# Optimization experiments

Measured on AMD Instinct MI355X. Metric: run time of the kernel, lower is better.

## Reference

```python
import jax, jax.numpy as jnp
import numpy as np

D_MODEL = 1024
N_HEADS = 16
HEAD_DIM = D_MODEL // N_HEADS
FFN_DIM = 4096
T = 2048
LN_EPS = 1e-5


def layer_norm(x, g, b):
    mu = jnp.mean(x, axis=-1, keepdims=True)
    var = jnp.mean(jnp.square(x - mu), axis=-1, keepdims=True)
    return (x - mu) * jax.lax.rsqrt(var + LN_EPS) * g + b


def setup_inputs() -> dict:
    key = jax.random.key(0)
    ks = jax.random.split(key, 12)
    s = 0.02
    x = jax.random.normal(ks[0], (1, T, D_MODEL), dtype=jnp.float32)
    # causal mask: True means masked (strict upper triangle)
    causal_mask = jnp.triu(jnp.ones((T, T), dtype=bool), k=1)
    # ALiBi bias: -slope * distance, per head
    slopes = 2.0 ** (-8.0 * (jnp.arange(1, N_HEADS + 1, dtype=jnp.float32) / N_HEADS))
    pos = jnp.arange(T, dtype=jnp.float32)
    dist = pos[None, :] - pos[:, None]  # (T, T)
    alibi_bias = slopes[:, None, None] * jnp.minimum(dist, 0.0)[None]  # (H, T, T)
    inp = {
        "x": x,
        "causal_mask": causal_mask,
        "alibi_bias": alibi_bias.astype(jnp.float32),
        "wq": jax.random.normal(ks[1], (D_MODEL, D_MODEL), jnp.float32) * s,
        "bq": jnp.zeros((D_MODEL,), jnp.float32),
        "wk": jax.random.normal(ks[2], (D_MODEL, D_MODEL), jnp.float32) * s,
        "bk": jnp.zeros((D_MODEL,), jnp.float32),
        "wv": jax.random.normal(ks[3], (D_MODEL, D_MODEL), jnp.float32) * s,
        "bv": jnp.zeros((D_MODEL,), jnp.float32),
        "wo": jax.random.normal(ks[4], (D_MODEL, D_MODEL), jnp.float32) * s,
        "bo": jnp.zeros((D_MODEL,), jnp.float32),
        "w1": jax.random.normal(ks[5], (D_MODEL, FFN_DIM), jnp.float32) * s,
        "b1": jnp.zeros((FFN_DIM,), jnp.float32),
        "w2": jax.random.normal(ks[6], (FFN_DIM, D_MODEL), jnp.float32) * s,
        "b2": jnp.zeros((D_MODEL,), jnp.float32),
        "g1": jnp.ones((D_MODEL,), jnp.float32),
        "be1": jnp.zeros((D_MODEL,), jnp.float32),
        "g2": jnp.ones((D_MODEL,), jnp.float32),
        "be2": jnp.zeros((D_MODEL,), jnp.float32),
    }
    return inp


def reference(x, causal_mask, alibi_bias, wq, bq, wk, bk, wv, bv, wo, bo,
              w1, b1, w2, b2, g1, be1, g2, be2):
    B, Tt, D = x.shape
    H, hd = N_HEADS, HEAD_DIM
    x_norm = layer_norm(x, g1, be1)
    # projections -> (B, H, T, hd)
    def split_heads(y):
        return y.reshape(B, Tt, H, hd).transpose(0, 2, 1, 3)
    Q = split_heads(x_norm @ wq + bq)
    K = split_heads(x_norm @ wk + bk)
    V = split_heads(x_norm @ wv + bv)
    scale = jnp.sqrt(jnp.float32(hd))
    scores = jnp.einsum('bhqd,bhkd->bhqk', Q, K) / scale
    scores = scores + alibi_bias[None]
    scores = jnp.where(causal_mask[None, None], -jnp.inf, scores)
    attn = jax.nn.softmax(scores, axis=-1)
    attn_out = jnp.einsum('bhqk,bhkd->bhqd', attn, V)
    attn_out = attn_out.transpose(0, 2, 1, 3).reshape(B, Tt, D)
    attn_out = attn_out @ wo + bo
    x = x + attn_out
    x_norm = layer_norm(x, g2, be2)
    h = jax.nn.gelu(x_norm @ w1 + b1, approximate=False)
    ffn_out = h @ w2 + b2
    return x + ffn_out
```

## Files before the change

kernel.cpp:

```cpp
#include <hip/hip_runtime.h>
#include <hip/hip_bf16.h>
#include <math.h>

#define T_SEQ 2048
#define D_MODEL 1024
#define N_HEADS 16
#define HEAD_DIM 64
#define FFN_DIM 4096

typedef _Float16 halfx8 __attribute__((ext_vector_type(8)));
typedef _Float16 halfx4 __attribute__((ext_vector_type(4)));
typedef float floatx4 __attribute__((ext_vector_type(4)));

__device__ __forceinline__ void async_ld16(const _Float16* g, _Float16* l) {
  __builtin_amdgcn_global_load_lds(
      (const __attribute__((address_space(1))) unsigned int*)g,
      (__attribute__((address_space(3))) unsigned int*)l, 16, 0, 0);
}

__global__ __launch_bounds__(256) void ln_h_kernel(
    const float* __restrict__ x, const float* __restrict__ g,
    const float* __restrict__ b, _Float16* __restrict__ y) {
  int row = blockIdx.x;
  const float* xr = x + (size_t)row * D_MODEL;
  _Float16* yr = y + (size_t)row * D_MODEL;
  int tid = threadIdx.x;
  int lid = tid & 63, wid = tid >> 6;
  __shared__ float red[8];

  float4 v = *(const float4*)&xr[tid * 4];
  float sum = v.x + v.y + v.z + v.w;
  for (int o = 32; o > 0; o >>= 1) sum += __shfl_down(sum, o, 64);
  if (lid == 0) red[wid] = sum;
  __syncthreads();
  if (tid == 0) { float t = 0; for (int i = 0; i < 4; i++) t += red[i]; red[0] = t; }
  __syncthreads();
  float mu = red[0] * (1.0f / D_MODEL);
  __syncthreads();

  float dx = v.x - mu, dy = v.y - mu, dz = v.z - mu, dw = v.w - mu;
  float vs = dx * dx + dy * dy + dz * dz + dw * dw;
  for (int o = 32; o > 0; o >>= 1) vs += __shfl_down(vs, o, 64);
  if (lid == 0) red[wid] = vs;
  __syncthreads();
  if (tid == 0) { float t = 0; for (int i = 0; i < 4; i++) t += red[i]; red[0] = t; }
  __syncthreads();
  float rstd = rsqrtf(red[0] * (1.0f / D_MODEL) + 1e-5f);

  float4 gv = *(const float4*)&g[tid * 4];
  float4 bv = *(const float4*)&b[tid * 4];
  halfx4 o;
  o[0] = (_Float16)(dx * rstd * gv.x + bv.x);
  o[1] = (_Float16)(dy * rstd * gv.y + bv.y);
  o[2] = (_Float16)(dz * rstd * gv.z + bv.z);
  o[3] = (_Float16)(dw * rstd * gv.w + bv.w);
  *(halfx4*)&yr[tid * 4] = o;
}

__global__ __launch_bounds__(256) void prep_kernel(
    const float* __restrict__ wq, const float* __restrict__ wk,
    const float* __restrict__ wv, const float* __restrict__ wo,
    const float* __restrict__ w1, const float* __restrict__ w2,
    const float* __restrict__ bq, const float* __restrict__ bk,
    const float* __restrict__ bv, _Float16* __restrict__ Wqkvt,
    _Float16* __restrict__ Wot, _Float16* __restrict__ W1t,
    _Float16* __restrict__ W2t, float* __restrict__ bqkv) {
  int bId = blockIdx.x;
  int tid = threadIdx.x;
  if (bId >= 12288) {
    int i = (bId - 12288) * 256 + tid;
    if (i < 1024) bqkv[i] = bq[i];
    else if (i < 2048) bqkv[i] = bk[i - 1024];
    else bqkv[i] = bv[i - 2048];
    return;
  }
  const float* in; _Float16* outp; int K, N, t;
  if (bId < 1024)      { in = wq; outp = Wqkvt;                 K = 1024; N = 1024; t = bId; }
  else if (bId < 2048) { in = wk; outp = Wqkvt + 1024 * 1024;   K = 1024; N = 1024; t = bId - 1024; }
  else if (bId < 3072) { in = wv; outp = Wqkvt + 2 * 1024 * 1024; K = 1024; N = 1024; t = bId - 2048; }
  else if (bId < 4096) { in = wo; outp = Wot;                   K = 1024; N = 1024; t = bId - 3072; }
  else if (bId < 8192) { in = w1; outp = W1t;                   K = 1024; N = 4096; t = bId - 4096; }
  else                 { in = w2; outp = W2t;                   K = 4096; N = 1024; t = bId - 8192; }
  int ntn = N / 32;
  int tk = (t / ntn) * 32, tn = (t % ntn) * 32;

  __shared__ float tile[32][33];
  int r = tid >> 3, c = (tid & 7) * 4;
  float4 v = *(const float4*)&in[(size_t)(tk + r) * N + tn + c];
  tile[r][c] = v.x; tile[r][c + 1] = v.y; tile[r][c + 2] = v.z; tile[r][c + 3] = v.w;
  __syncthreads();
  halfx4 o;
  o[0] = (_Float16)tile[c][r];
  o[1] = (_Float16)tile[c + 1][r];
  o[2] = (_Float16)tile[c + 2][r];
  o[3] = (_Float16)tile[c + 3][r];
  *(halfx4*)&outp[(size_t)(tn + r) * K + tk + c] = o;
}

template <int MODE, int BM_>
__global__ __launch_bounds__(256) void hgemm_kernel(
    const _Float16* __restrict__ A, const _Float16* __restrict__ Bt,
    const float* __restrict__ bias, const float* __restrict__ res,
    float* __restrict__ Cf, _Float16* __restrict__ Ch,
    _Float16* __restrict__ Vtg, int M, int N, int K) {
  constexpr int TM = BM_ / 32;
  __shared__ _Float16 As[BM_][32];
  __shared__ _Float16 Bs[128][32];
  const int tid = threadIdx.x;
  const int w = tid >> 6, lane = tid & 63;
  const int l16 = lane & 15, quad = lane >> 4;
  const int m0 = blockIdx.y * BM_, n0 = blockIdx.x * 128;
  const int wm = (w >> 1) * (BM_ / 2), wn = (w & 1) * 64;

  floatx4 acc[TM][4];
#pragma unroll
  for (int i = 0; i < TM; i++)
#pragma unroll
    for (int j = 0; j < 4; j++) acc[i][j] = (floatx4){0.f, 0.f, 0.f, 0.f};

  const int srow = lane >> 2;
  const int scol = (lane & 3) * 8;
  const _Float16* Ag;
  _Float16* AsB;
  if (BM_ == 128) { Ag = A + (size_t)(m0 + w * 32 + srow) * K + scol; AsB = &As[w * 32][0]; }
  else            { Ag = A + (size_t)(m0 + w * 16 + srow) * K + scol; AsB = &As[w * 16][0]; }
  const _Float16* Bg = Bt + (size_t)(n0 + w * 32 + srow) * K + scol;
  _Float16* BsB = &Bs[w * 32][0];

  for (int k0 = 0; k0 < K; k0 += 32) {
    async_ld16(Ag + k0, AsB);
    if (BM_ == 128) async_ld16(Ag + k0 + (size_t)16 * K, AsB + 16 * 32);
    async_ld16(Bg + k0, BsB);
    async_ld16(Bg + k0 + (size_t)16 * K, BsB + 16 * 32);
    __syncthreads();
    halfx8 af[TM], bf[4];
#pragma unroll
    for (int mt = 0; mt < TM; mt++) af[mt] = *(const halfx8*)&As[wm + mt * 16 + l16][quad * 8];
#pragma unroll
    for (int nt = 0; nt < 4; nt++) bf[nt] = *(const halfx8*)&Bs[wn + nt * 16 + l16][quad * 8];
#pragma unroll
    for (int mt = 0; mt < TM; mt++)
#pragma unroll
      for (int nt = 0; nt < 4; nt++)
        acc[mt][nt] = __builtin_amdgcn_mfma_f32_16x16x32_f16(af[mt], bf[nt], acc[mt][nt], 0, 0, 0);
    __syncthreads();
  }

#pragma unroll
  for (int mt = 0; mt < TM; mt++) {
    int row0 = m0 + wm + mt * 16 + quad * 4;
#pragma unroll
    for (int nt = 0; nt < 4; nt++) {
      int col = n0 + wn + nt * 16 + l16;
      float bv = bias[col];
      float vv[4];
#pragma unroll
      for (int r = 0; r < 4; r++) {
        float v = acc[mt][nt][r] + bv;
        if (MODE == 1) v = 0.5f * v * (1.0f + erff(v * 0.70710678118f));
        vv[r] = v;
      }
      if (MODE == 2) {
#pragma unroll
        for (int r = 0; r < 4; r++)
          Cf[(size_t)(row0 + r) * N + col] = vv[r] + res[(size_t)(row0 + r) * N + col];
      } else if (MODE == 3) {
        if (col < 2048) {
#pragma unroll
          for (int r = 0; r < 4; r++)
            Ch[(size_t)(row0 + r) * 2048 + col] = (_Float16)vv[r];
        } else {
          halfx4 pk;
#pragma unroll
          for (int r = 0; r < 4; r++) pk[r] = (_Float16)vv[r];
          *(halfx4*)&Vtg[(size_t)(col - 2048) * T_SEQ + row0] = pk;
        }
      } else {
#pragma unroll
        for (int r = 0; r < 4; r++)
          Ch[(size_t)(row0 + r) * N + col] = (_Float16)vv[r];
      }
    }
  }
}

#define LROW 72
__global__ __launch_bounds__(256) void flash_attn_kernel(
    const _Float16* __restrict__ QK, const _Float16* __restrict__ Vtg,
    _Float16* __restrict__ out) {
  __shared__ _Float16 Ks[64][LROW];
  __shared__ _Float16 Vt[64][LROW];
  __shared__ _Float16 Ps[4][16][LROW];

  const int h = blockIdx.y;
  const int qt = blockIdx.x;
  const int q0 = qt * 64;
  const int tid = threadIdx.x;
  const int w = tid >> 6;
  const int lane = tid & 63;
  const int l16 = lane & 15;
  const int quad = lane >> 4;

  const _Float16* Qg = QK + h * HEAD_DIM;
  const _Float16* Kg = QK + 1024 + h * HEAD_DIM;
  const _Float16* Vg = Vtg + (size_t)h * HEAD_DIM * T_SEQ;

  const _Float16* qp = Qg + (size_t)(q0 + w * 16 + l16) * 2048;
  halfx8 qa0 = *(const halfx8*)(qp + quad * 8);
  halfx8 qa1 = *(const halfx8*)(qp + 32 + quad * 8);

  float m_i[4], l_i[4];
  floatx4 o_acc[4];
#pragma unroll
  for (int r = 0; r < 4; r++) { m_i[r] = -INFINITY; l_i[r] = 0.f; }
#pragma unroll
  for (int c = 0; c < 4; c++) o_acc[c] = (floatx4){0.f, 0.f, 0.f, 0.f};

  const float scale2 = 0.18033688f;
  const float slope2 = exp2f(-0.5f * (float)(h + 1)) * 1.44269504f;
  const int row_base = q0 + w * 16 + quad * 4;

  const int kr = tid >> 3;
  const int c8 = tid & 7;
  halfx8 kpre0, kpre1, vpre0, vpre1;
#define PREFETCH(K0)                                                          \
  {                                                                           \
    kpre0 = *(const halfx8*)(Kg + (size_t)((K0) + kr) * 2048 + c8 * 8);       \
    kpre1 = *(const halfx8*)(Kg + (size_t)((K0) + kr + 32) * 2048 + c8 * 8);  \
    vpre0 = *(const halfx8*)(Vg + (size_t)kr * T_SEQ + (K0) + c8 * 8);        \
    vpre1 = *(const halfx8*)(Vg + (size_t)(kr + 32) * T_SEQ + (K0) + c8 * 8); \
  }
  PREFETCH(0)

  for (int t = 0; t <= qt; t++) {
    const int k0 = t * 64;
    __syncthreads();
    *(halfx8*)&Ks[kr][c8 * 8] = kpre0;
    *(halfx8*)&Ks[kr + 32][c8 * 8] = kpre1;
    *(halfx8*)&Vt[kr][((c8 ^ (kr >> 3)) & 7) * 8] = vpre0;
    *(halfx8*)&Vt[kr + 32][((c8 ^ ((kr + 32) >> 3)) & 7) * 8] = vpre1;
    __syncthreads();
    if (t < qt) PREFETCH(k0 + 64)

    float sc[4][4];
#pragma unroll
    for (int sub = 0; sub < 4; sub++) {
      halfx8 b0 = *(const halfx8*)(&Ks[sub * 16 + l16][quad * 8]);
      halfx8 b1 = *(const halfx8*)(&Ks[sub * 16 + l16][32 + quad * 8]);
      floatx4 acc = (floatx4){0.f, 0.f, 0.f, 0.f};
      acc = __builtin_amdgcn_mfma_f32_16x16x32_f16(qa0, b0, acc, 0, 0, 0);
      acc = __builtin_amdgcn_mfma_f32_16x16x32_f16(qa1, b1, acc, 0, 0, 0);
#pragma unroll
      for (int r = 0; r < 4; r++) sc[sub][r] = acc[r];
    }

#pragma unroll
    for (int r = 0; r < 4; r++) {
      const int rg = row_base + r;
      float mx = m_i[r];
#pragma unroll
      for (int sub = 0; sub < 4; sub++) {
        int cg = k0 + sub * 16 + l16;
        float s = sc[sub][r] * scale2 + slope2 * (float)(cg - rg);
        if (cg > rg) s = -1e30f;
        sc[sub][r] = s;
        mx = fmaxf(mx, s);
      }
      mx = fmaxf(mx, __shfl_xor(mx, 1, 64));
      mx = fmaxf(mx, __shfl_xor(mx, 2, 64));
      mx = fmaxf(mx, __shfl_xor(mx, 4, 64));
      mx = fmaxf(mx, __shfl_xor(mx, 8, 64));
      float alpha = exp2f(m_i[r] - mx);
      m_i[r] = mx;
      float ls = 0.f;
#pragma unroll
      for (int sub = 0; sub < 4; sub++) {
        float p = exp2f(sc[sub][r] - mx);
        ls += p;
        Ps[w][quad * 4 + r][sub * 16 + l16] = (_Float16)p;
      }
      ls += __shfl_xor(ls, 1, 64);
      ls += __shfl_xor(ls, 2, 64);
      ls += __shfl_xor(ls, 4, 64);
      ls += __shfl_xor(ls, 8, 64);
      l_i[r] = l_i[r] * alpha + ls;
#pragma unroll
      for (int c = 0; c < 4; c++) o_acc[c][r] *= alpha;
    }

#pragma unroll
    for (int kh = 0; kh < 2; kh++) {
      halfx8 pa = *(const halfx8*)(&Ps[w][l16][kh * 32 + quad * 8]);
      int kgrp = kh * 4 + quad;
#pragma unroll
      for (int c = 0; c < 4; c++) {
        int d = c * 16 + l16;
        halfx8 vb = *(const halfx8*)(&Vt[d][((kgrp ^ (d >> 3)) & 7) << 3]);
        o_acc[c] = __builtin_amdgcn_mfma_f32_16x16x32_f16(pa, vb, o_acc[c], 0, 0, 0);
      }
    }
  }

#pragma unroll
  for (int c = 0; c < 4; c++)
#pragma unroll
    for (int r = 0; r < 4; r++)
      out[(size_t)(row_base + r) * D_MODEL + h * HEAD_DIM + c * 16 + l16] =
          (_Float16)(o_acc[c][r] / l_i[r]);
}

extern "C" void kernel_launch(void* const* d_in, const int* in_sizes, int n_in,
                              void* d_out, int out_size, void* d_ws, size_t ws_size,
                              hipStream_t stream) {
  const float* x   = (const float*)d_in[0];
  const float* wq  = (const float*)d_in[3];
  const float* bq  = (const float*)d_in[4];
  const float* wk  = (const float*)d_in[5];
  const float* bk  = (const float*)d_in[6];
  const float* wv  = (const float*)d_in[7];
  const float* bv  = (const float*)d_in[8];
  const float* wo  = (const float*)d_in[9];
  const float* bo  = (const float*)d_in[10];
  const float* w1  = (const float*)d_in[11];
  const float* b1  = (const float*)d_in[12];
  const float* w2  = (const float*)d_in[13];
  const float* b2  = (const float*)d_in[14];
  const float* g1  = (const float*)d_in[15];
  const float* be1 = (const float*)d_in[16];
  const float* g2  = (const float*)d_in[17];
  const float* be2 = (const float*)d_in[18];
  float* out = (float*)d_out;

  const size_t TD = (size_t)T_SEQ * D_MODEL;
  char* p = (char*)d_ws;
  float*    x1    = (float*)p;     p += TD * 4;
  float*    bqkv  = (float*)p;     p += 4096 * 4;
  _Float16* xnh   = (_Float16*)p;  p += TD * 2;
  _Float16* QKh   = (_Float16*)p;  p += (size_t)2048 * 2048 * 2;
  _Float16* Vtg   = (_Float16*)p;  p += (size_t)1024 * 2048 * 2;
  _Float16* attnh = (_Float16*)p;  p += TD * 2;
  _Float16* hh    = (_Float16*)p;  p += (size_t)2048 * 4096 * 2;
  _Float16* Wqkvt = (_Float16*)p;  p += (size_t)3 * 1024 * 1024 * 2;
  _Float16* Wot   = (_Float16*)p;  p += (size_t)1024 * 1024 * 2;
  _Float16* W1t   = (_Float16*)p;  p += (size_t)1024 * 4096 * 2;
  _Float16* W2t   = (_Float16*)p;  p += (size_t)4096 * 1024 * 2;

  dim3 blk(256);

  prep_kernel<<<dim3(12300), blk, 0, stream>>>(wq, wk, wv, wo, w1, w2, bq, bk, bv,
                                               Wqkvt, Wot, W1t, W2t, bqkv);

  ln_h_kernel<<<T_SEQ, blk, 0, stream>>>(x, g1, be1, xnh);

  hgemm_kernel<3, 128><<<dim3(3072 / 128, T_SEQ / 128), blk, 0, stream>>>(
      xnh, Wqkvt, bqkv, nullptr, nullptr, QKh, Vtg, T_SEQ, 3072, 1024);

  flash_attn_kernel<<<dim3(T_SEQ / 64, N_HEADS), blk, 0, stream>>>(QKh, Vtg, attnh);

  hgemm_kernel<2, 64><<<dim3(1024 / 128, T_SEQ / 64), blk, 0, stream>>>(
      attnh, Wot, bo, x, x1, nullptr, nullptr, T_SEQ, 1024, 1024);

  ln_h_kernel<<<T_SEQ, blk, 0, stream>>>(x1, g2, be2, xnh);

  hgemm_kernel<1, 128><<<dim3(4096 / 128, T_SEQ / 128), blk, 0, stream>>>(
      xnh, W1t, b1, nullptr, nullptr, hh, nullptr, T_SEQ, 4096, 1024);

  hgemm_kernel<2, 64><<<dim3(1024 / 128, T_SEQ / 64), blk, 0, stream>>>(
      hh, W2t, b2, x1, out, nullptr, nullptr, T_SEQ, 1024, 4096);
}
```

Before: 599.2 us.

## Double-buffer GEMM and attention LDS tiles with async loads and swizzling

The GEMM kernel now keeps two LDS buffers per operand. The next k-tile is issued with global_load_lds before computing the current one, which removes one barrier per iteration, and an XOR swizzle is meant to avoid bank conflicts. Flash attention gets the same treatment: K/V are loaded asynchronously into double-buffered, swizzled LDS instead of going through register prefetch. It also launches the longest causal q-tiles first and applies the causal mask only on diagonal tiles. The GEMM tiles shrink to 64x128 and 64x64 to raise block counts, at the cost of less reuse per block and more LDS per block.

```diff
diff --git a/kernel.cpp b/kernel.cpp
--- a/kernel.cpp
+++ b/kernel.cpp
@@ -97,60 +97,70 @@
   *(halfx4*)&outp[(size_t)(tn + r) * K + tk + c] = o;
 }
 
-template <int MODE, int BM_>
+template <int MODE, int BM, int BN>
 __global__ __launch_bounds__(256) void hgemm_kernel(
     const _Float16* __restrict__ A, const _Float16* __restrict__ Bt,
     const float* __restrict__ bias, const float* __restrict__ res,
     float* __restrict__ Cf, _Float16* __restrict__ Ch,
     _Float16* __restrict__ Vtg, int M, int N, int K) {
-  constexpr int TM = BM_ / 32;
-  __shared__ _Float16 As[BM_][32];
-  __shared__ _Float16 Bs[128][32];
+  constexpr int TM = BM / 32;
+  constexpr int TN = BN / 32;
+  constexpr int AR = BM / 64;
+  constexpr int BR = BN / 64;
+  __shared__ _Float16 As[2][BM][32];
+  __shared__ _Float16 Bs[2][BN][32];
   const int tid = threadIdx.x;
   const int w = tid >> 6, lane = tid & 63;
   const int l16 = lane & 15, quad = lane >> 4;
-  const int m0 = blockIdx.y * BM_, n0 = blockIdx.x * 128;
-  const int wm = (w >> 1) * (BM_ / 2), wn = (w & 1) * 64;
-
-  floatx4 acc[TM][4];
+  const int m0 = blockIdx.y * BM, n0 = blockIdx.x * BN;
+  const int wm = (w >> 1) * (BM / 2), wn = (w & 1) * (BN / 2);
+
+  floatx4 acc[TM][TN];
 #pragma unroll
   for (int i = 0; i < TM; i++)
 #pragma unroll
-    for (int j = 0; j < 4; j++) acc[i][j] = (floatx4){0.f, 0.f, 0.f, 0.f};
-
-  const int srow = lane >> 2;
-  const int scol = (lane & 3) * 8;
-  const _Float16* Ag;
-  _Float16* AsB;
-  if (BM_ == 128) { Ag = A + (size_t)(m0 + w * 32 + srow) * K + scol; AsB = &As[w * 32][0]; }
-  else            { Ag = A + (size_t)(m0 + w * 16 + srow) * K + scol; AsB = &As[w * 16][0]; }
-  const _Float16* Bg = Bt + (size_t)(n0 + w * 32 + srow) * K + scol;
-  _Float16* BsB = &Bs[w * 32][0];
-
-  for (int k0 = 0; k0 < K; k0 += 32) {
-    async_ld16(Ag + k0, AsB);
-    if (BM_ == 128) async_ld16(Ag + k0 + (size_t)16 * K, AsB + 16 * 32);
-    async_ld16(Bg + k0, BsB);
-    async_ld16(Bg + k0 + (size_t)16 * K, BsB + 16 * 32);
+    for (int j = 0; j < TN; j++) acc[i][j] = (floatx4){0.f, 0.f, 0.f, 0.f};
+
+  const int srow = w * 16 + (lane >> 2);
+  const int gg = (lane & 3) ^ ((srow >> 1) & 3);
+  const _Float16* Agp = A + (size_t)(m0 + srow) * K + gg * 8;
+  const _Float16* Bgp = Bt + (size_t)(n0 + srow) * K + gg * 8;
+
+  const int colA = (quad ^ ((l16 >> 1) & 3)) * 8;
+
+  const int NIT = K / 32;
+#define HG_ISSUE(buf, k0)                                                     \
+  {                                                                           \
+    _Pragma("unroll") for (int i = 0; i < AR; i++)                            \
+        async_ld16(Agp + (k0) + (size_t)i * 64 * K, &As[buf][i * 64 + w * 16][0]); \
+    _Pragma("unroll") for (int i = 0; i < BR; i++)                            \
+        async_ld16(Bgp + (k0) + (size_t)i * 64 * K, &Bs[buf][i * 64 + w * 16][0]); \
+  }
+  HG_ISSUE(0, 0)
+
+  for (int it = 0; it < NIT; it++) {
     __syncthreads();
-    halfx8 af[TM], bf[4];
-#pragma unroll
-    for (int mt = 0; mt < TM; mt++) af[mt] = *(const halfx8*)&As[wm + mt * 16 + l16][quad * 8];
-#pragma unroll
-    for (int nt = 0; nt < 4; nt++) bf[nt] = *(const halfx8*)&Bs[wn + nt * 16 + l16][quad * 8];
+    if (it + 1 < NIT) HG_ISSUE((it + 1) & 1, (it + 1) * 32)
+    const int buf = it & 1;
+    halfx8 af[TM], bf[TN];
 #pragma unroll
     for (int mt = 0; mt < TM; mt++)
-#pragma unroll
-      for (int nt = 0; nt < 4; nt++)
+      af[mt] = *(const halfx8*)&As[buf][wm + mt * 16 + l16][colA];
+#pragma unroll
+    for (int nt = 0; nt < TN; nt++)
+      bf[nt] = *(const halfx8*)&Bs[buf][wn + nt * 16 + l16][colA];
+#pragma unroll
+    for (int mt = 0; mt < TM; mt++)
+#pragma unroll
+      for (int nt = 0; nt < TN; nt++)
         acc[mt][nt] = __builtin_amdgcn_mfma_f32_16x16x32_f16(af[mt], bf[nt], acc[mt][nt], 0, 0, 0);
-    __syncthreads();
   }
 
 #pragma unroll
   for (int mt = 0; mt < TM; mt++) {
     int row0 = m0 + wm + mt * 16 + quad * 4;
 #pragma unroll
-    for (int nt = 0; nt < 4; nt++) {
+    for (int nt = 0; nt < TN; nt++) {
       int col = n0 + wn + nt * 16 + l16;
       float bv = bias[col];
       float vv[4];
@@ -188,12 +198,12 @@
 __global__ __launch_bounds__(256) void flash_attn_kernel(
     const _Float16* __restrict__ QK, const _Float16* __restrict__ Vtg,
     _Float16* __restrict__ out) {
-  __shared__ _Float16 Ks[64][LROW];
-  __shared__ _Float16 Vt[64][LROW];
+  __shared__ _Float16 Ks[2][64][64];
+  __shared__ _Float16 Vt[2][64][64];
   __shared__ _Float16 Ps[4][16][LROW];
 
   const int h = blockIdx.y;
-  const int qt = blockIdx.x;
+  const int qt = 31 - blockIdx.x;
   const int q0 = qt * 64;
   const int tid = threadIdx.x;
   const int w = tid >> 6;
@@ -220,33 +230,38 @@
   const float slope2 = exp2f(-0.5f * (float)(h + 1)) * 1.44269504f;
   const int row_base = q0 + w * 16 + quad * 4;
 
-  const int kr = tid >> 3;
-  const int c8 = tid & 7;
-  halfx8 kpre0, kpre1, vpre0, vpre1;
-#define PREFETCH(K0)                                                          \
-  {                                                                           \
-    kpre0 = *(const halfx8*)(Kg + (size_t)((K0) + kr) * 2048 + c8 * 8);       \
-    kpre1 = *(const halfx8*)(Kg + (size_t)((K0) + kr + 32) * 2048 + c8 * 8);  \
-    vpre0 = *(const halfx8*)(Vg + (size_t)kr * T_SEQ + (K0) + c8 * 8);        \
-    vpre1 = *(const halfx8*)(Vg + (size_t)(kr + 32) * T_SEQ + (K0) + c8 * 8); \
-  }
-  PREFETCH(0)
+  const int sr = w * 8 + (lane >> 3);
+  const int gg = (lane & 7) ^ ((lane >> 3) & 7);
+  const _Float16* Kp = Kg + (size_t)sr * 2048 + gg * 8;
+  const _Float16* Vp = Vg + (size_t)sr * 2048 + gg * 8;
+
+  const int m7 = l16 & 7;
+  const int cK0 = (quad ^ m7) * 8;
+  const int cK1 = cK0 ^ 32;
+  const int cV0 = (quad ^ m7) * 8;
+  const int cV1 = ((quad + 4) ^ m7) * 8;
+
+#define FA_ISSUE(buf, k0)                                                      \
+  {                                                                            \
+    async_ld16(Kp + (size_t)(k0) * 2048, &Ks[buf][w * 8][0]);                  \
+    async_ld16(Kp + (size_t)((k0) + 32) * 2048, &Ks[buf][32 + w * 8][0]);      \
+    async_ld16(Vp + (k0), &Vt[buf][w * 8][0]);                                 \
+    async_ld16(Vp + (size_t)32 * 2048 + (k0), &Vt[buf][32 + w * 8][0]);        \
+  }
+  FA_ISSUE(0, 0)
 
   for (int t = 0; t <= qt; t++) {
     const int k0 = t * 64;
+    const int buf = t & 1;
     __syncthreads();
-    *(halfx8*)&Ks[kr][c8 * 8] = kpre0;
-    *(halfx8*)&Ks[kr + 32][c8 * 8] = kpre1;
-    *(halfx8*)&Vt[kr][((c8 ^ (kr >> 3)) & 7) * 8] = vpre0;
-    *(halfx8*)&Vt[kr + 32][((c8 ^ ((kr + 32) >> 3)) & 7) * 8] = vpre1;
-    __syncthreads();
-    if (t < qt) PREFETCH(k0 + 64)
+    if (t < qt) FA_ISSUE(buf ^ 1, k0 + 64)
 
     float sc[4][4];
 #pragma unroll
     for (int sub = 0; sub < 4; sub++) {
-      halfx8 b0 = *(const halfx8*)(&Ks[sub * 16 + l16][quad * 8]);
-      halfx8 b1 = *(const halfx8*)(&Ks[sub * 16 + l16][32 + quad * 8]);
+      const _Float16* kr = &Ks[buf][sub * 16 + l16][0];
+      halfx8 b0 = *(const halfx8*)(kr + cK0);
+      halfx8 b1 = *(const halfx8*)(kr + cK1);
       floatx4 acc = (floatx4){0.f, 0.f, 0.f, 0.f};
       acc = __builtin_amdgcn_mfma_f32_16x16x32_f16(qa0, b0, acc, 0, 0, 0);
       acc = __builtin_amdgcn_mfma_f32_16x16x32_f16(qa1, b1, acc, 0, 0, 0);
@@ -254,6 +269,7 @@
       for (int r = 0; r < 4; r++) sc[sub][r] = acc[r];
     }
 
+    const bool diag = (t == qt);
 #pragma unroll
     for (int r = 0; r < 4; r++) {
       const int rg = row_base + r;
@@ -262,7 +278,7 @@
       for (int sub = 0; sub < 4; sub++) {
         int cg = k0 + sub * 16 + l16;
         float s = sc[sub][r] * scale2 + slope2 * (float)(cg - rg);
-        if (cg > rg) s = -1e30f;
+        if (diag && cg > rg) s = -1e30f;
         sc[sub][r] = s;
         mx = fmaxf(mx, s);
       }
@@ -291,11 +307,10 @@
 #pragma unroll
     for (int kh = 0; kh < 2; kh++) {
       halfx8 pa = *(const halfx8*)(&Ps[w][l16][kh * 32 + quad * 8]);
-      int kgrp = kh * 4 + quad;
+      const int cV = kh ? cV1 : cV0;
 #pragma unroll
       for (int c = 0; c < 4; c++) {
-        int d = c * 16 + l16;
-        halfx8 vb = *(const halfx8*)(&Vt[d][((kgrp ^ (d >> 3)) & 7) << 3]);
+        halfx8 vb = *(const halfx8*)(&Vt[buf][c * 16 + l16][cV]);
         o_acc[c] = __builtin_amdgcn_mfma_f32_16x16x32_f16(pa, vb, o_acc[c], 0, 0, 0);
       }
     }
@@ -352,19 +367,19 @@
 
   ln_h_kernel<<<T_SEQ, blk, 0, stream>>>(x, g1, be1, xnh);
 
-  hgemm_kernel<3, 128><<<dim3(3072 / 128, T_SEQ / 128), blk, 0, stream>>>(
+  hgemm_kernel<3, 64, 128><<<dim3(3072 / 128, T_SEQ / 64), blk, 0, stream>>>(
       xnh, Wqkvt, bqkv, nullptr, nullptr, QKh, Vtg, T_SEQ, 3072, 1024);
 
   flash_attn_kernel<<<dim3(T_SEQ / 64, N_HEADS), blk, 0, stream>>>(QKh, Vtg, attnh);
 
-  hgemm_kernel<2, 64><<<dim3(1024 / 128, T_SEQ / 64), blk, 0, stream>>>(
+  hgemm_kernel<2, 64, 64><<<dim3(1024 / 64, T_SEQ / 64), blk, 0, stream>>>(
       attnh, Wot, bo, x, x1, nullptr, nullptr, T_SEQ, 1024, 1024);
 
   ln_h_kernel<<<T_SEQ, blk, 0, stream>>>(x1, g2, be2, xnh);
 
-  hgemm_kernel<1, 128><<<dim3(4096 / 128, T_SEQ / 128), blk, 0, stream>>>(
+  hgemm_kernel<1, 64, 128><<<dim3(4096 / 128, T_SEQ / 64), blk, 0, stream>>>(
       xnh, W1t, b1, nullptr, nullptr, hh, nullptr, T_SEQ, 4096, 1024);
 
-  hgemm_kernel<2, 64><<<dim3(1024 / 128, T_SEQ / 64), blk, 0, stream>>>(
+  hgemm_kernel<2, 64, 64><<<dim3(1024 / 64, T_SEQ / 64), blk, 0, stream>>>(
       hh, W2t, b2, x1, out, nullptr, nullptr, T_SEQ, 1024, 4096);
 }
```

Result: faster. 568.8 us (-5.1%).
